# Optimization experiments

Hardware: AMD Instinct MI355X
Metric: run time of the kernel (lower is better)

The kernel has to match this reference:

```python
import jax, jax.numpy as jnp
import numpy as np
from jax import lax

LEAK = 0.2
EPS = 1e-5
T = 20  # sequence_length


def _lrelu(x):
    return jnp.where(x >= 0, x, LEAK * x)


def _deconv(x, w, stride=2, k=4, p=1):
    # PyTorch ConvTranspose2d(weight [in,out,kH,kW], stride=2, pad=1) equivalent:
    # flip kernel spatially, swap in/out channels, use lhs_dilation.
    wt = jnp.flip(w, (2, 3)).transpose(1, 0, 2, 3)  # OIHW
    pad = k - 1 - p
    return lax.conv_general_dilated(
        x, wt, window_strides=(1, 1), padding=[(pad, pad), (pad, pad)],
        lhs_dilation=(stride, stride),
        dimension_numbers=('NCHW', 'OIHW', 'NCHW'))


def _bn(x, g, b):
    # BatchNorm2d, training mode (batch statistics, biased variance)
    m = x.mean((0, 2, 3), keepdims=True)
    v = x.var((0, 2, 3), keepdims=True)
    return (x - m) * lax.rsqrt(v + EPS) * g[None, :, None, None] + b[None, :, None, None]


def setup_inputs() -> dict:
    B, CD, MD, H, FF = 64, 128, 128, 256, 512
    ks = jax.random.split(jax.random.key(0), 32)
    rn = lambda k, sh, s=0.02: (s * jax.random.normal(k, sh)).astype(jnp.float32)
    return {
        'z_content': jax.random.normal(ks[0], (B, CD), jnp.float32),
        'z_motion': jax.random.normal(ks[1], (B, MD), jnp.float32),
        'W_h': rn(ks[2], (H, CD + MD)), 'b_h': jnp.zeros((H,), jnp.float32),
        'W_c': rn(ks[3], (H, CD + MD)), 'b_c': jnp.zeros((H,), jnp.float32),
        'W_ih': rn(ks[4], (4 * H, H)), 'W_hh': rn(ks[5], (4 * H, H)),
        'b_ih': jnp.zeros((4 * H,), jnp.float32), 'b_hh': jnp.zeros((4 * H,), jnp.float32),
        'W_f': rn(ks[6], (FF, H)), 'b_f': jnp.zeros((FF,), jnp.float32),
        'init_in': rn(ks[7], (1, H), 0.1),
        'fc_W': rn(ks[8], (256 * 4 * 4, FF + CD)), 'fc_b': jnp.zeros((256 * 16,), jnp.float32),
        'w0': rn(ks[9], (256, 128, 4, 4)), 'g0': jnp.ones((128,), jnp.float32), 'be0': jnp.zeros((128,), jnp.float32),
        'w1': rn(ks[10], (128, 64, 4, 4)), 'g1': jnp.ones((64,), jnp.float32), 'be1': jnp.zeros((64,), jnp.float32),
        'w2': rn(ks[11], (64, 32, 4, 4)), 'g2': jnp.ones((32,), jnp.float32), 'be2': jnp.zeros((32,), jnp.float32),
        'wf': rn(ks[12], (32, 1, 4, 4)), 'bf': jnp.zeros((1,), jnp.float32),
    }


def reference(z_content, z_motion, W_h, b_h, W_c, b_c, W_ih, W_hh, b_ih, b_hh,
              W_f, b_f, init_in, fc_W, fc_b, w0, g0, be0, w1, g1, be1,
              w2, g2, be2, wf, bf):
    B = z_content.shape[0]
    z = jnp.concatenate([z_content, z_motion], axis=-1)
    h0 = z @ W_h.T + b_h  # [B,H]
    c0 = z @ W_c.T + b_c
    x0 = jnp.broadcast_to(init_in, (B, init_in.shape[1]))
    bias = b_ih + b_hh

    def step(carry, _):
        x, h, c = carry
        gates = x @ W_ih.T + h @ W_hh.T + bias  # [B,4H], torch gate order i,f,g,o
        i, f, g, o = jnp.split(gates, 4, axis=-1)
        c_new = jax.nn.sigmoid(f) * c + jax.nn.sigmoid(i) * jnp.tanh(g)
        h_new = jax.nn.sigmoid(o) * jnp.tanh(c_new)
        return (h_new, h_new, c_new), h_new

    _, outs = lax.scan(step, (x0, h0, c0), None, length=T)  # [T,B,H]
    outs = outs.transpose(1, 0, 2)  # [B,T,H]

    ff = _lrelu(outs @ W_f.T + b_f)  # [B,T,FF]
    zc = jnp.broadcast_to(z_content[:, None, :], (B, T, z_content.shape[1]))
    feat = jnp.concatenate([ff, zc], axis=-1).reshape(B * T, -1)  # [B*T, FF+CD]

    h = _lrelu(feat @ fc_W.T + fc_b).reshape(B * T, 256, 4, 4)
    h = _lrelu(_bn(_deconv(h, w0), g0, be0))   # [B*T,128,8,8]
    h = _lrelu(_bn(_deconv(h, w1), g1, be1))   # [B*T,64,16,16]
    h = _lrelu(_bn(_deconv(h, w2), g2, be2))   # [B*T,32,32,32]
    out = jax.nn.sigmoid(_deconv(h, wf) + bf[None, :, None, None])  # [B*T,1,64,64]
    return out.reshape(B, T, *out.shape[1:])
```

## Files before the change

kernel.cpp:

```cpp
#include <hip/hip_runtime.h>
#include <hip/hip_bf16.h>
#include <math.h>

typedef __hip_bfloat16 bf16;
typedef __attribute__((ext_vector_type(8))) short bf16x8;
typedef __attribute__((ext_vector_type(4))) float f32x4;
typedef __attribute__((ext_vector_type(2))) float f32x2;

#define LRELU(v) ((v) > 0.f ? (v) : 0.2f*(v))

__device__ __forceinline__ float sig_f(float x){ return 1.f/(1.f + __expf(-x)); }
__device__ __forceinline__ float tanh_f(float x){
  float ax = fabsf(x);
  float e = __expf(-2.f*ax);
  float t = (1.f - e)/(1.f + e);
  return x >= 0.f ? t : -t;
}
__device__ __forceinline__ ushort bfbits(float v){
  bf16 b = __float2bfloat16(v);
  return *(ushort*)&b;
}
__device__ __forceinline__ uint bfpack(float a, float b){
  return (uint)bfbits(a) | ((uint)bfbits(b) << 16);
}
__device__ __forceinline__ float bflo(uint u){ return __uint_as_float(u << 16); }
__device__ __forceinline__ float bfhi(uint u){ return __uint_as_float(u & 0xffff0000u); }

__global__ void k_tobf16(const float* __restrict__ src, ushort* __restrict__ dst, int n){
  int i = blockIdx.x*256 + threadIdx.x;
  if (i < n) dst[i] = bfbits(src[i]);
}

__global__ void k_transpose(const float* __restrict__ src, float* __restrict__ dst, int R, int C){
  __shared__ float t[32][33];
  int c0 = blockIdx.x*32, r0 = blockIdx.y*32;
  int tx = threadIdx.x, ty = threadIdx.y;
  #pragma unroll
  for (int i = 0; i < 4; ++i)
    t[ty+8*i][tx] = src[(size_t)(r0+ty+8*i)*C + c0+tx];
  __syncthreads();
  #pragma unroll
  for (int i = 0; i < 4; ++i)
    dst[(size_t)(c0+ty+8*i)*R + r0+tx] = t[tx][ty+8*i];
}

__global__ void k_w4prep(const float* __restrict__ Wih, const float* __restrict__ Whh,
                         uint4* __restrict__ Whq8, uint4* __restrict__ Wsq8,
                         float* __restrict__ stats){
  int k4 = blockIdx.x, j = threadIdx.x;
  if (k4 < 2) { int i = k4*256 + j; if (i < 448) stats[i] = 0.f; }
  uint h4[4], s4[4];
  #pragma unroll
  for (int d = 0; d < 4; ++d) {
    int k = 4*k4 + d;
    float hi = Whh[j*256+k],       hf = Whh[(256+j)*256+k];
    float hg = Whh[(512+j)*256+k], ho = Whh[(768+j)*256+k];
    float ii = Wih[j*256+k],       iff = Wih[(256+j)*256+k];
    float ig = Wih[(512+j)*256+k], io = Wih[(768+j)*256+k];
    int lo = __builtin_amdgcn_cvt_pk_fp8_f32(hi, hf, 0, false);
    h4[d] = (uint)__builtin_amdgcn_cvt_pk_fp8_f32(hg, ho, lo, true);
    lo = __builtin_amdgcn_cvt_pk_fp8_f32(hi+ii, hf+iff, 0, false);
    s4[d] = (uint)__builtin_amdgcn_cvt_pk_fp8_f32(hg+ig, ho+io, lo, true);
  }
  Whq8[k4*256+j] = make_uint4(h4[0], h4[1], h4[2], h4[3]);
  Wsq8[k4*256+j] = make_uint4(s4[0], s4[1], s4[2], s4[3]);
}

__global__ void k_xgbias(const float* __restrict__ Wih, const float* __restrict__ b_ih,
                         const float* __restrict__ b_hh, const float* __restrict__ init_in,
                         float4* __restrict__ xg4, float4* __restrict__ bias4){
  int b = blockIdx.x, t = threadIdx.x;
  float v = init_in[t];
  float p0 = v * Wih[b*256 + t];
  float p1 = v * Wih[(256+b)*256 + t];
  float p2 = v * Wih[(512+b)*256 + t];
  float p3 = v * Wih[(768+b)*256 + t];
  #pragma unroll
  for (int o = 32; o; o >>= 1) {
    p0 += __shfl_xor(p0, o); p1 += __shfl_xor(p1, o);
    p2 += __shfl_xor(p2, o); p3 += __shfl_xor(p3, o);
  }
  __shared__ float4 red[4];
  int lane = t & 63, wid = t >> 6;
  if (lane == 0) red[wid] = make_float4(p0,p1,p2,p3);
  __syncthreads();
  if (t == 0) {
    float4 bi = make_float4(b_ih[b]+b_hh[b], b_ih[256+b]+b_hh[256+b],
                            b_ih[512+b]+b_hh[512+b], b_ih[768+b]+b_hh[768+b]);
    bias4[b] = bi;
    float4 a = bi;
    #pragma unroll
    for (int w = 0; w < 4; ++w) { a.x += red[w].x; a.y += red[w].y; a.z += red[w].z; a.w += red[w].w; }
    xg4[b] = a;
  }
}

__global__ __launch_bounds__(256) void k_h0c0(const float* __restrict__ zc, const float* __restrict__ zm,
                      const float* __restrict__ WhT, const float* __restrict__ WcT,
                      const float* __restrict__ b_h, const float* __restrict__ b_c,
                      float* __restrict__ h, float* __restrict__ c){
  __shared__ float zs[256];
  int b = blockIdx.x, j = threadIdx.x;
  zs[j] = (j < 128) ? zc[b*128 + j] : zm[b*128 + (j-128)];
  __syncthreads();
  float ah = b_h[j], ac = b_c[j];
  #pragma unroll 4
  for (int k = 0; k < 256; ++k) {
    float zv = zs[k];
    ah = fmaf(zv, WhT[k*256 + j], ah);
    ac = fmaf(zv, WcT[k*256 + j], ac);
  }
  h[b*256+j] = ah; c[b*256+j] = ac;
}

__global__ __launch_bounds__(1024) void k_lstm_all(
    const uint4* __restrict__ Whq8, const uint4* __restrict__ Wsq8,
    const float4* __restrict__ xg4, const float4* __restrict__ bias4,
    const float* __restrict__ h0, const float* __restrict__ c0,
    ushort* __restrict__ outsb){
  __shared__ float hs[256];
  __shared__ float4 part[3][256];
  const int b = blockIdx.x, tid = threadIdx.x;
  const int j = tid & 255, kq = tid >> 8;
  float cj = 0.f;
  if (kq == 0) { hs[j] = h0[b*256 + j]; cj = c0[b*256 + j]; }
  __syncthreads();
  for (int t = 0; t < 20; ++t) {
    const uint4* __restrict__ Wp = ((t == 0) ? Whq8 : Wsq8) + (size_t)(kq*16)*256 + j;
    float4 a = make_float4(0.f, 0.f, 0.f, 0.f);
    #pragma unroll 8
    for (int kk = 0; kk < 16; ++kk) {
      uint4 wv = Wp[(size_t)kk*256];
      const float* __restrict__ hb = &hs[kq*64 + 4*kk];
      {
        f32x2 pif = __builtin_amdgcn_cvt_pk_f32_fp8((int)wv.x, false);
        f32x2 pgo = __builtin_amdgcn_cvt_pk_f32_fp8((int)wv.x, true);
        float hv = hb[0];
        a.x = fmaf(hv, pif[0], a.x); a.y = fmaf(hv, pif[1], a.y);
        a.z = fmaf(hv, pgo[0], a.z); a.w = fmaf(hv, pgo[1], a.w);
      }
      {
        f32x2 pif = __builtin_amdgcn_cvt_pk_f32_fp8((int)wv.y, false);
        f32x2 pgo = __builtin_amdgcn_cvt_pk_f32_fp8((int)wv.y, true);
        float hv = hb[1];
        a.x = fmaf(hv, pif[0], a.x); a.y = fmaf(hv, pif[1], a.y);
        a.z = fmaf(hv, pgo[0], a.z); a.w = fmaf(hv, pgo[1], a.w);
      }
      {
        f32x2 pif = __builtin_amdgcn_cvt_pk_f32_fp8((int)wv.z, false);
        f32x2 pgo = __builtin_amdgcn_cvt_pk_f32_fp8((int)wv.z, true);
        float hv = hb[2];
        a.x = fmaf(hv, pif[0], a.x); a.y = fmaf(hv, pif[1], a.y);
        a.z = fmaf(hv, pgo[0], a.z); a.w = fmaf(hv, pgo[1], a.w);
      }
      {
        f32x2 pif = __builtin_amdgcn_cvt_pk_f32_fp8((int)wv.w, false);
        f32x2 pgo = __builtin_amdgcn_cvt_pk_f32_fp8((int)wv.w, true);
        float hv = hb[3];
        a.x = fmaf(hv, pif[0], a.x); a.y = fmaf(hv, pif[1], a.y);
        a.z = fmaf(hv, pgo[0], a.z); a.w = fmaf(hv, pgo[1], a.w);
      }
    }
    if (kq) part[kq-1][j] = a;
    __syncthreads();
    if (kq == 0) {
      float4 p1 = part[0][j], p2 = part[1][j], p3 = part[2][j];
      float4 bb = (t == 0) ? xg4[j] : bias4[j];
      a.x += p1.x + p2.x + p3.x + bb.x;
      a.y += p1.y + p2.y + p3.y + bb.y;
      a.z += p1.z + p2.z + p3.z + bb.z;
      a.w += p1.w + p2.w + p3.w + bb.w;
      float ig = sig_f(a.x), fg = sig_f(a.y), gg = tanh_f(a.z), og = sig_f(a.w);
      cj = fmaf(fg, cj, ig*gg);
      float hj = og * tanh_f(cj);
      outsb[(b*20 + t)*256 + j] = bfbits(hj);
      hs[j] = hj;
    }
    __syncthreads();
  }
}

__global__ void k_zc(const float* __restrict__ zc, ushort* __restrict__ featb){
  int e = blockIdx.x*256 + threadIdx.x;
  int r = e >> 7, c = e & 127;
  featb[r*640 + 512 + c] = bfbits(zc[(r/20)*128 + c]);
}

__global__ __launch_bounds__(256) void k_ff_m(
    const ushort* __restrict__ A, const ushort* __restrict__ W,
    const float* __restrict__ bias, ushort* __restrict__ C)
{
  constexpr int K = 256, BK = 64, NK = K/BK, BM = 128, BN = 64;
  constexpr int RS = 72;
  constexpr int NCF = BN/16;
  constexpr int AC = 4, WC = 2;

  __shared__ __align__(16) ushort Al[2][BM*RS];
  __shared__ __align__(16) ushort Wl[2][BN*RS];

  const int tid = threadIdx.x;
  const int col0 = blockIdx.x * BN, row0 = blockIdx.y * BM;
  const int w = tid >> 6, l = tid & 63, lm = l & 15, lk = l >> 4;

  f32x4 acc[NCF][2];
  #pragma unroll
  for (int m = 0; m < NCF; ++m)
    #pragma unroll
    for (int s = 0; s < 2; ++s)
      acc[m][s] = (f32x4){0.f,0.f,0.f,0.f};

  uint4 ar[AC], wr[WC];

  #define LOADG(kt) { \
    _Pragma("unroll") \
    for (int i = 0; i < AC; ++i) { \
      int chunk = tid + i*256; \
      int rl = chunk >> 3, kc = chunk & 7; \
      ar[i] = *(const uint4*)&A[(size_t)(row0+rl)*K + (kt)*BK + kc*8]; \
    } \
    _Pragma("unroll") \
    for (int i = 0; i < WC; ++i) { \
      int chunk = tid + i*256; \
      int co = chunk >> 3, kc = chunk & 7; \
      wr[i] = *(const uint4*)&W[(size_t)(col0+co)*K + (kt)*BK + kc*8]; \
    } }

  #define STOREL(buf) { \
    _Pragma("unroll") \
    for (int i = 0; i < AC; ++i) { \
      int chunk = tid + i*256; \
      int rl = chunk >> 3, kc = chunk & 7; \
      *(uint4*)&Al[buf][rl*RS + kc*8] = ar[i]; \
    } \
    _Pragma("unroll") \
    for (int i = 0; i < WC; ++i) { \
      int chunk = tid + i*256; \
      int co = chunk >> 3, kc = chunk & 7; \
      *(uint4*)&Wl[buf][co*RS + kc*8] = wr[i]; \
    } }

  LOADG(0);
  STOREL(0);
  int cur = 0;
  for (int kt = 0; kt < NK; ++kt) {
    if (kt + 1 < NK) LOADG(kt + 1);
    __syncthreads();
    #pragma unroll
    for (int kf = 0; kf < 2; ++kf) {
      bf16x8 bfr[2];
      #pragma unroll
      for (int s = 0; s < 2; ++s)
        bfr[s] = *(bf16x8*)&Al[cur][(w*32 + s*16 + lm)*RS + kf*32 + lk*8];
      #pragma unroll
      for (int m = 0; m < NCF; ++m) {
        bf16x8 afr = *(bf16x8*)&Wl[cur][(m*16 + lm)*RS + kf*32 + lk*8];
        acc[m][0] = __builtin_amdgcn_mfma_f32_16x16x32_bf16(afr, bfr[0], acc[m][0], 0, 0, 0);
        acc[m][1] = __builtin_amdgcn_mfma_f32_16x16x32_bf16(afr, bfr[1], acc[m][1], 0, 0, 0);
      }
    }
    if (kt + 1 < NK) STOREL(cur ^ 1);
    cur ^= 1;
  }

  #pragma unroll
  for (int m = 0; m < NCF; ++m) {
    #pragma unroll
    for (int s = 0; s < 2; ++s) {
      int row = row0 + w*32 + s*16 + lm;
      f32x4 v = acc[m][s];
      int u0 = col0 + m*16 + lk*4;
      union { ushort u[4]; uint2 q; } pk;
      #pragma unroll
      for (int j = 0; j < 4; ++j)
        pk.u[j] = bfbits(LRELU(v[j] + bias[u0+j]));
      *(uint2*)&C[(size_t)row*640 + u0] = pk.q;
    }
  }
  #undef LOADG
  #undef STOREL
}

__global__ __launch_bounds__(256) void k_gemm_fc_m(
    const ushort* __restrict__ A, const ushort* __restrict__ W,
    const float* __restrict__ bias, ushort* __restrict__ C)
{
  constexpr int K = 640, BK = 64, NK = K/BK, BM = 128, BN = 64;
  constexpr int RS = 72;
  constexpr int NCF = BN/16;
  constexpr int AC = 4, WC = 2;

  __shared__ __align__(16) ushort Al[2][BM*RS];
  __shared__ __align__(16) ushort Wl[2][BN*RS];

  const int tid = threadIdx.x;
  const int col0 = blockIdx.x * BN, row0 = blockIdx.y * BM;
  const int w = tid >> 6, l = tid & 63, lm = l & 15, lk = l >> 4;

  f32x4 acc[NCF][2];
  #pragma unroll
  for (int m = 0; m < NCF; ++m)
    #pragma unroll
    for (int s = 0; s < 2; ++s)
      acc[m][s] = (f32x4){0.f,0.f,0.f,0.f};

  uint4 ar[AC], wr[WC];

  #define LOADG(kt) { \
    _Pragma("unroll") \
    for (int i = 0; i < AC; ++i) { \
      int chunk = tid + i*256; \
      int rl = chunk >> 3, kc = chunk & 7; \
      ar[i] = *(const uint4*)&A[(size_t)(row0+rl)*K + (kt)*BK + kc*8]; \
    } \
    _Pragma("unroll") \
    for (int i = 0; i < WC; ++i) { \
      int chunk = tid + i*256; \
      int co = chunk >> 3, kc = chunk & 7; \
      wr[i] = *(const uint4*)&W[(size_t)(col0+co)*K + (kt)*BK + kc*8]; \
    } }

  #define STOREL(buf) { \
    _Pragma("unroll") \
    for (int i = 0; i < AC; ++i) { \
      int chunk = tid + i*256; \
      int rl = chunk >> 3, kc = chunk & 7; \
      *(uint4*)&Al[buf][rl*RS + kc*8] = ar[i]; \
    } \
    _Pragma("unroll") \
    for (int i = 0; i < WC; ++i) { \
      int chunk = tid + i*256; \
      int co = chunk >> 3, kc = chunk & 7; \
      *(uint4*)&Wl[buf][co*RS + kc*8] = wr[i]; \
    } }

  LOADG(0);
  STOREL(0);
  int cur = 0;
  for (int kt = 0; kt < NK; ++kt) {
    if (kt + 1 < NK) LOADG(kt + 1);
    __syncthreads();
    #pragma unroll
    for (int kf = 0; kf < 2; ++kf) {
      bf16x8 bfr[2];
      #pragma unroll
      for (int s = 0; s < 2; ++s)
        bfr[s] = *(bf16x8*)&Al[cur][(w*32 + s*16 + lm)*RS + kf*32 + lk*8];
      #pragma unroll
      for (int m = 0; m < NCF; ++m) {
        bf16x8 afr = *(bf16x8*)&Wl[cur][(m*16 + lm)*RS + kf*32 + lk*8];
        acc[m][0] = __builtin_amdgcn_mfma_f32_16x16x32_bf16(afr, bfr[0], acc[m][0], 0, 0, 0);
        acc[m][1] = __builtin_amdgcn_mfma_f32_16x16x32_bf16(afr, bfr[1], acc[m][1], 0, 0, 0);
      }
    }
    if (kt + 1 < NK) STOREL(cur ^ 1);
    cur ^= 1;
  }

  #pragma unroll
  for (int m = 0; m < NCF; ++m) {
    #pragma unroll
    for (int s = 0; s < 2; ++s) {
      int row = row0 + w*32 + s*16 + lm;
      f32x4 v = acc[m][s];
      #pragma unroll
      for (int j = 0; j < 4; ++j) {
        int u = col0 + m*16 + lk*4 + j;
        float val = LRELU(v[j] + bias[u]);
        C[((size_t)row << 12) + ((size_t)(u & 15) << 8) + (u >> 4)] = bfbits(val);
      }
    }
  }
  #undef LOADG
  #undef STOREL
}

template<int CI, int CO>
__global__ void k_wprep_im(const float* __restrict__ w, ushort* __restrict__ wpn){
  constexpr int K = 4*CI, KF = K/32, MMW2 = CO/16;
  int e = blockIdx.x*256 + threadIdx.x;
  if (e >= 16*CI*CO) return;
  int j  = e & 7;
  int lk = (e >> 3) & 3;
  int lm = (e >> 5) & 15;
  int r3 = e >> 9;
  int kf = r3 % KF; int r4 = r3 / KF;
  int m  = r4 % MMW2; int p = r4 / MMW2;
  int k  = kf*32 + lk*8 + j;
  int t  = k / CI, ci = k % CI;
  int co = m*16 + lm;
  int py = p >> 1, px = p & 1, dy = t >> 1, dx = t & 1;
  int ky = (py ? 0 : 1) + 2*dy;
  int kx = (px ? 0 : 1) + 2*dx;
  wpn[e] = bfbits(w[((ci*CO + co)*4 + ky)*4 + kx]);
}

__global__ void k_wfprep(const float* __restrict__ wf, ushort* __restrict__ wfb){
  int e = blockIdx.x*256 + threadIdx.x;
  if (e < 512) {
    int t = e >> 5, ci = e & 31;
    wfb[t*32 + ci] = bfbits(wf[ci*16 + t]);
  }
}

template<int CI, int CO, int HI>
__global__ __launch_bounds__(256) void k_dcv(
    const ushort* __restrict__ in, const ushort* __restrict__ wp,
    ushort* __restrict__ out, float* __restrict__ gsum, float* __restrict__ gsq)
{
  constexpr int WI = HI, HO = 2*HI, WO = 2*WI;
  constexpr int K = 4*CI, BK = 64, NK = K/BK, KFT = K/32;
  constexpr int BSP = 128;
  constexpr int RS = 72;
  constexpr int NCF = CO/32;
  constexpr int COH = CO/2;
  constexpr int AC = BSP/32;

  __shared__ __align__(16) ushort Al[2][BSP*RS];
  __shared__ float s_sum[COH], s_sq[COH];

  const int tid = threadIdx.x;
  const int sp0 = blockIdx.x * BSP;
  const int p  = blockIdx.y;
  const int coz = blockIdx.z;
  const int py = p >> 1, px = p & 1;
  const int w  = tid >> 6, l = tid & 63;
  const int lm = l & 15, lk = l >> 4;

  if (tid < COH) { s_sum[tid] = 0.f; s_sq[tid] = 0.f; }

  f32x4 acc[NCF][2];
  #pragma unroll
  for (int m = 0; m < NCF; ++m)
    #pragma unroll
    for (int s = 0; s < 2; ++s)
      acc[m][s] = (f32x4){0.f,0.f,0.f,0.f};

  uint4 ar[AC];
  const ushort* wpb = wp + (size_t)(p*(CO/16) + coz*NCF)*KFT*512;

  #define LOADT(kt) { \
    int t = ((kt)*BK)/CI, ci0 = ((kt)*BK)%CI; \
    int dy = t >> 1, dx = t & 1; \
    _Pragma("unroll") \
    for (int i = 0; i < AC; ++i) { \
      int chunk = tid + i*256; \
      int rl = chunk >> 3, kc = chunk & 7; \
      int r = sp0 + rl; \
      int n = r / (HI*WI), rem = r % (HI*WI); \
      int oy = rem / WI, ox = rem % WI; \
      int iy = oy + py - dy, ix = ox + px - dx; \
      if ((unsigned)iy < (unsigned)HI && (unsigned)ix < (unsigned)WI) \
        ar[i] = *(const uint4*)&in[((((size_t)n*HI + iy)*WI + ix)*CI) + ci0 + kc*8]; \
      else ar[i] = make_uint4(0,0,0,0); \
    } }

  #define STORET(buf) { \
    _Pragma("unroll") \
    for (int i = 0; i < AC; ++i) { \
      int chunk = tid + i*256; \
      int rl = chunk >> 3, kc = chunk & 7; \
      *(uint4*)&Al[buf][rl*RS + kc*8] = ar[i]; \
    } }

  LOADT(0);
  STORET(0);
  int cur = 0;
  for (int kt = 0; kt < NK; ++kt) {
    if (kt + 1 < NK) LOADT(kt + 1);
    __syncthreads();
    #pragma unroll
    for (int kf = 0; kf < 2; ++kf) {
      const int ktg = kt*2 + kf;
      bf16x8 bfr[2];
      #pragma unroll
      for (int s = 0; s < 2; ++s)
        bfr[s] = *(bf16x8*)&Al[cur][(w*32 + s*16 + lm)*RS + kf*32 + lk*8];
      #pragma unroll
      for (int m = 0; m < NCF; ++m) {
        bf16x8 afr = *(const bf16x8*)&wpb[((size_t)m*KFT + ktg)*512 + lm*32 + lk*8];
        acc[m][0] = __builtin_amdgcn_mfma_f32_16x16x32_bf16(afr, bfr[0], acc[m][0], 0, 0, 0);
        acc[m][1] = __builtin_amdgcn_mfma_f32_16x16x32_bf16(afr, bfr[1], acc[m][1], 0, 0, 0);
      }
    }
    if (kt + 1 < NK) STORET(cur ^ 1);
    cur ^= 1;
  }

  #pragma unroll
  for (int m = 0; m < NCF; ++m) {
    float s1[4] = {0,0,0,0}, s2[4] = {0,0,0,0};
    #pragma unroll
    for (int s = 0; s < 2; ++s) {
      f32x4 v = acc[m][s];
      #pragma unroll
      for (int j = 0; j < 4; ++j) { s1[j] += v[j]; s2[j] += v[j]*v[j]; }
    }
    #pragma unroll
    for (int j = 0; j < 4; ++j) {
      float a = s1[j], b = s2[j];
      #pragma unroll
      for (int o = 1; o < 16; o <<= 1) { a += __shfl_xor(a, o); b += __shfl_xor(b, o); }
      if (lm == 0) {
        atomicAdd(&s_sum[m*16 + lk*4 + j], a);
        atomicAdd(&s_sq [m*16 + lk*4 + j], b);
      }
    }
  }
  #pragma unroll
  for (int s = 0; s < 2; ++s) {
    int sp = sp0 + w*32 + s*16 + lm;
    int n = sp / (HI*WI), rem = sp % (HI*WI);
    int y = 2*(rem / WI) + py, x = 2*(rem % WI) + px;
    size_t ob = (((size_t)n*HO + y)*WO + x)*CO + coz*COH + lk*4;
    #pragma unroll
    for (int m = 0; m < NCF; ++m) {
      f32x4 v = acc[m][s];
      union { ushort u[4]; uint2 q; } pk;
      pk.u[0] = bfbits(v[0]); pk.u[1] = bfbits(v[1]);
      pk.u[2] = bfbits(v[2]); pk.u[3] = bfbits(v[3]);
      *(uint2*)&out[ob + m*16] = pk.q;
    }
  }
  __syncthreads();
  for (int cc = tid; cc < COH; cc += 256) {
    atomicAdd(&gsum[coz*COH + cc], s_sum[cc]);
    atomicAdd(&gsq[coz*COH + cc],  s_sq[cc]);
  }
  #undef LOADT
  #undef STORET
}

template<int CI, int CO, int HI>
__global__ __launch_bounds__(512) void k_dcvim(
    const ushort* __restrict__ in, const ushort* __restrict__ wp,
    const float* __restrict__ gsumP, const float* __restrict__ gsqP,
    const float* __restrict__ gP, const float* __restrict__ beP, float invNP,
    ushort* __restrict__ out, float* __restrict__ gsum, float* __restrict__ gsq)
{
  constexpr int WI = HI, HO = 2*HI, WO = 2*WI;
  constexpr int K = 4*CI;
  constexpr int KF = K/32;
  constexpr int PAD = HI + 2;
  constexpr int CICH = CI/8;
  constexpr int MMW2 = CO/16;
  constexpr int SFTH = HI*WI/32;

  __shared__ __align__(16) ushort Ain[PAD*PAD*CI];
  __shared__ float s_sum[CO], s_sq[CO];
  __shared__ float s_scale[CI], s_shift[CI];

  const int tid = threadIdx.x;
  const int n = blockIdx.x;
  const int w = tid >> 6, l = tid & 63, lm = l & 15, lk = l >> 4;
  const int p = w >> 1, py = p >> 1, px = p & 1, ph = w & 1;

  if (tid < CO) { s_sum[tid] = 0.f; s_sq[tid] = 0.f; }
  if (tid >= 512-CI) {
    int c = tid - (512-CI);
    float m = gsumP[c]*invNP;
    float v = gsqP[c]*invNP - m*m;
    float sc = gP[c]*rsqrtf(v + 1e-5f);
    s_scale[c] = sc;
    s_shift[c] = beP[c] - m*sc;
  }
  __syncthreads();

  const ushort* inb = in + (size_t)n * HI * WI * CI;
  constexpr int NPCH = PAD*PAD*CICH;
  for (int e = tid; e < NPCH; e += 512) {
    int ci8 = e % CICH; int sp = e / CICH;
    int c = sp % PAD, r = sp / PAD;
    int chS = ci8 ^ (c & 7);
    if (r >= 1 && r <= HI && c >= 1 && c <= WI) {
      uint4 u = *(const uint4*)&inb[(((size_t)(r-1)*WI + (c-1))*CI) + ci8*8];
      int ci0 = ci8*8;
      float4 sc0 = *(const float4*)&s_scale[ci0];
      float4 sc1 = *(const float4*)&s_scale[ci0+4];
      float4 sh0 = *(const float4*)&s_shift[ci0];
      float4 sh1 = *(const float4*)&s_shift[ci0+4];
      float v0 = LRELU(fmaf(bflo(u.x), sc0.x, sh0.x));
      float v1 = LRELU(fmaf(bfhi(u.x), sc0.y, sh0.y));
      float v2 = LRELU(fmaf(bflo(u.y), sc0.z, sh0.z));
      float v3 = LRELU(fmaf(bfhi(u.y), sc0.w, sh0.w));
      float v4 = LRELU(fmaf(bflo(u.z), sc1.x, sh1.x));
      float v5 = LRELU(fmaf(bfhi(u.z), sc1.y, sh1.y));
      float v6 = LRELU(fmaf(bflo(u.w), sc1.z, sh1.z));
      float v7 = LRELU(fmaf(bfhi(u.w), sc1.w, sh1.w));
      uint4 o;
      o.x = (uint)bfpack(v0, v1);
      o.y = (uint)bfpack(v2, v3);
      o.z = (uint)bfpack(v4, v5);
      o.w = (uint)bfpack(v6, v7);
      ((uint4*)Ain)[(r*PAD + c)*CICH + chS] = o;
    } else {
      ((uint4*)Ain)[(r*PAD + c)*CICH + chS] = make_uint4(0,0,0,0);
    }
  }
  __syncthreads();

  f32x4 acc[MMW2][SFTH];
  #pragma unroll
  for (int m = 0; m < MMW2; ++m)
    #pragma unroll
    for (int sf = 0; sf < SFTH; ++sf)
      acc[m][sf] = (f32x4){0.f,0.f,0.f,0.f};

  const ushort* wpb = wp + (size_t)(p*MMW2)*KF*512;
  #pragma unroll
  for (int kf = 0; kf < KF; ++kf) {
    const int t = (kf*32)/CI, cib = (kf*32)%CI;
    const int dy = t >> 1, dx = t & 1;
    bf16x8 afr[MMW2];
    #pragma unroll
    for (int m = 0; m < MMW2; ++m)
      afr[m] = *(const bf16x8*)&wpb[((size_t)m*KF + kf)*512 + lm*32 + lk*8];
    const int ch = (cib >> 3) + lk;
    #pragma unroll
    for (int sf = 0; sf < SFTH; ++sf) {
      int s = (ph*SFTH + sf)*16 + lm;
      int y = s / WI, x = s % WI;
      int r = y + py - dy + 1, c = x + px - dx + 1;
      bf16x8 bfr = *(const bf16x8*)&Ain[((r*PAD + c)*CICH + (ch ^ (c & 7)))*8];
      #pragma unroll
      for (int m = 0; m < MMW2; ++m)
        acc[m][sf] = __builtin_amdgcn_mfma_f32_16x16x32_bf16(afr[m], bfr, acc[m][sf], 0, 0, 0);
    }
  }

  float s1[MMW2][4], s2[MMW2][4];
  #pragma unroll
  for (int m = 0; m < MMW2; ++m)
    #pragma unroll
    for (int j = 0; j < 4; ++j) { s1[m][j] = 0.f; s2[m][j] = 0.f; }

  #pragma unroll
  for (int sf = 0; sf < SFTH; ++sf) {
    int s = (ph*SFTH + sf)*16 + lm;
    int y = 2*(s / WI) + py, x = 2*(s % WI) + px;
    size_t ob = (((size_t)n*HO + y)*WO + x)*CO + lk*4;
    #pragma unroll
    for (int m = 0; m < MMW2; ++m) {
      f32x4 v = acc[m][sf];
      union { ushort u[4]; uint2 q; } pk;
      #pragma unroll
      for (int j = 0; j < 4; ++j) {
        pk.u[j] = bfbits(v[j]);
        s1[m][j] += v[j];
        s2[m][j] += v[j]*v[j];
      }
      *(uint2*)&out[ob + m*16] = pk.q;
    }
  }

  #pragma unroll
  for (int m = 0; m < MMW2; ++m) {
    #pragma unroll
    for (int j = 0; j < 4; ++j) {
      float a = s1[m][j], b = s2[m][j];
      #pragma unroll
      for (int o = 1; o < 16; o <<= 1) { a += __shfl_xor(a, o); b += __shfl_xor(b, o); }
      if (lm == 0) {
        atomicAdd(&s_sum[m*16 + lk*4 + j], a);
        atomicAdd(&s_sq [m*16 + lk*4 + j], b);
      }
    }
  }

  __syncthreads();
  for (int cc = tid; cc < CO; cc += 512) {
    atomicAdd(&gsum[cc], s_sum[cc]);
    atomicAdd(&gsq[cc],  s_sq[cc]);
  }
}

__global__ __launch_bounds__(256) void k_final(
    const ushort* __restrict__ in, const ushort* __restrict__ wfb,
    const float* __restrict__ gsumP, const float* __restrict__ gsqP,
    const float* __restrict__ gP, const float* __restrict__ beP, float invNP,
    const float* __restrict__ bfb, float* __restrict__ outp)
{
  constexpr int CI=32, HI=32, WI=32, HO=64, WO=64, SPLIT=4, HOq=HO/SPLIT;
  constexpr int RMAX = 10;
  constexpr int DP = 20;
  __shared__ float Dl[RMAX*32*DP];
  __shared__ float s_scale[CI], s_shift[CI];

  const int tid = threadIdx.x, bid = blockIdx.x;
  const int n = bid % 1280, q = bid / 1280;
  const int y0 = q * HOq;
  const int rows_lo = max(0, y0/2 - 1);
  const int rows_hi = min(HI-1, (y0 + HOq)/2);
  const int nrows = rows_hi - rows_lo + 1;

  if (tid < CI) {
    float m = gsumP[tid]*invNP;
    float v = gsqP[tid]*invNP - m*m;
    float sc = gP[tid]*rsqrtf(v + 1e-5f);
    s_scale[tid] = sc;
    s_shift[tid] = beP[tid] - m*sc;
  }
  __syncthreads();

  const int w = tid >> 6, l = tid & 63, lm = l & 15, lk = l >> 4;
  const bf16x8 afr = *(const bf16x8*)&wfb[lm*32 + lk*8];
  const float4 sc0 = *(const float4*)&s_scale[lk*8];
  const float4 sc1 = *(const float4*)&s_scale[lk*8+4];
  const float4 sh0 = *(const float4*)&s_shift[lk*8];
  const float4 sh1 = *(const float4*)&s_shift[lk*8+4];

  const ushort* inb = in + (size_t)n * HI * WI * CI;
  const int ngrp = nrows * 2;
  for (int g = w; g < ngrp; g += 4) {
    int px = g*16 + lm;
    int rl = px >> 5, ix = px & 31;
    uint4 u = *(const uint4*)&inb[(((size_t)(rows_lo+rl)*WI + ix)*CI) + lk*8];
    float v0 = LRELU(fmaf(bflo(u.x), sc0.x, sh0.x));
    float v1 = LRELU(fmaf(bfhi(u.x), sc0.y, sh0.y));
    float v2 = LRELU(fmaf(bflo(u.y), sc0.z, sh0.z));
    float v3 = LRELU(fmaf(bfhi(u.y), sc0.w, sh0.w));
    float v4 = LRELU(fmaf(bflo(u.z), sc1.x, sh1.x));
    float v5 = LRELU(fmaf(bfhi(u.z), sc1.y, sh1.y));
    float v6 = LRELU(fmaf(bflo(u.w), sc1.z, sh1.z));
    float v7 = LRELU(fmaf(bfhi(u.w), sc1.w, sh1.w));
    union { uint uu[4]; bf16x8 v; } pk;
    pk.uu[0] = bfpack(v0, v1);
    pk.uu[1] = bfpack(v2, v3);
    pk.uu[2] = bfpack(v4, v5);
    pk.uu[3] = bfpack(v6, v7);
    f32x4 d = __builtin_amdgcn_mfma_f32_16x16x32_bf16(afr, pk.v, (f32x4){0.f,0.f,0.f,0.f}, 0, 0, 0);
    *(f32x4*)&Dl[px*DP + lk*4] = d;
  }
  __syncthreads();

  const float b0 = bfb[0];
  #pragma unroll
  for (int i = 0; i < (HOq*WO)/256; ++i) {
    int e = tid + i*256;
    int oy = e >> 6, x = e & 63;
    int y = y0 + oy;
    int kya = (y + 1) & 1, iya = (y + 1) >> 1;
    int kxa = (x + 1) & 1, ixa = (x + 1) >> 1;
    float acc = b0;
    #pragma unroll
    for (int dy = 0; dy < 2; ++dy) {
      int iy = iya - dy, ky = kya + 2*dy;
      if (iy < 0 || iy >= HI) continue;
      #pragma unroll
      for (int dx = 0; dx < 2; ++dx) {
        int ix = ixa - dx, kx = kxa + 2*dx;
        if (ix < 0 || ix >= WI) continue;
        acc += Dl[((iy - rows_lo)*WI + ix)*DP + (ky*4 + kx)];
      }
    }
    outp[(size_t)n*HO*WO + y*WO + x] = 1.f/(1.f + __expf(-acc));
  }
}

extern "C" void kernel_launch(void* const* d_in, const int* in_sizes, int n_in,
                              void* d_out, int out_size, void* d_ws, size_t ws_size,
                              hipStream_t stream) {
  const float* z_content = (const float*)d_in[0];
  const float* z_motion  = (const float*)d_in[1];
  const float* W_h  = (const float*)d_in[2];
  const float* b_h  = (const float*)d_in[3];
  const float* W_c  = (const float*)d_in[4];
  const float* b_c  = (const float*)d_in[5];
  const float* W_ih = (const float*)d_in[6];
  const float* W_hh = (const float*)d_in[7];
  const float* b_ih = (const float*)d_in[8];
  const float* b_hh = (const float*)d_in[9];
  const float* W_f  = (const float*)d_in[10];
  const float* b_f  = (const float*)d_in[11];
  const float* init_in = (const float*)d_in[12];
  const float* fc_W = (const float*)d_in[13];
  const float* fc_b = (const float*)d_in[14];
  const float* w0 = (const float*)d_in[15];
  const float* g0 = (const float*)d_in[16];
  const float* be0 = (const float*)d_in[17];
  const float* w1 = (const float*)d_in[18];
  const float* g1 = (const float*)d_in[19];
  const float* be1 = (const float*)d_in[20];
  const float* w2 = (const float*)d_in[21];
  const float* g2 = (const float*)d_in[22];
  const float* be2 = (const float*)d_in[23];
  const float* wf = (const float*)d_in[24];
  const float* bf_ = (const float*)d_in[25];

  const size_t P_BYTES = 10631168;
  const size_t X_OFF   = P_BYTES;
  const size_t X_BYTES = 83886080;
  const size_t Y_OFF   = X_OFF + X_BYTES;
  const size_t NEED    = Y_OFF + 41943040;
  if (ws_size < NEED) return;

  float* ws = (float*)d_ws;
  char*  wsb = (char*)d_ws;
  float* sum0 = ws + 0;        float* sq0 = ws + 128;
  float* sum1 = ws + 256;      float* sq1 = ws + 320;
  float* sum2 = ws + 384;      float* sq2 = ws + 416;
  float4* xg4   = (float4*)(ws + 1024);
  float4* bias4 = (float4*)(ws + 2048);
  float* h    = ws + 3072;
  float* c    = ws + 19456;
  ushort* outsb = (ushort*)(ws + 35840);
  float* WhT  = ws + 199680;
  float* WcT  = ws + 265216;
  uint4* Whq8 = (uint4*)(ws + 330752);
  uint4* Wsq8 = (uint4*)(ws + 592896);
  ushort* wp0 = (ushort*)(ws + 855040);
  ushort* wp1 = (ushort*)(ws + 1117184);
  ushort* wp2 = (ushort*)(ws + 1182720);
  ushort* wfb = (ushort*)(ws + 1199104);
  ushort* wpff = (ushort*)(ws + 1199616);
  ushort* featb = (ushort*)(ws + 1265152);

  ushort* wpfc = (ushort*)(wsb + X_OFF);
  ushort* out0 = (ushort*)(wsb + X_OFF);
  ushort* out2 = (ushort*)(wsb + X_OFF);
  ushort* h1   = (ushort*)(wsb + Y_OFF);
  ushort* out1 = (ushort*)(wsb + Y_OFF);

  dim3 tb(32,8);
  k_transpose<<<dim3(8,8),   tb, 0, stream>>>(W_h,  WhT, 256, 256);
  k_transpose<<<dim3(8,8),   tb, 0, stream>>>(W_c,  WcT, 256, 256);
  k_tobf16<<<10240, 256, 0, stream>>>(fc_W, wpfc, 2621440);
  k_tobf16<<<512, 256, 0, stream>>>(W_f, wpff, 131072);
  k_w4prep<<<64, 256, 0, stream>>>(W_ih, W_hh, Whq8, Wsq8, ws);
  k_xgbias<<<256, 256, 0, stream>>>(W_ih, b_ih, b_hh, init_in, xg4, bias4);
  k_h0c0<<<64, 256, 0, stream>>>(z_content, z_motion, WhT, WcT, b_h, b_c, h, c);
  k_wprep_im<256,128><<<2048, 256, 0, stream>>>(w0, wp0);
  k_wprep_im<128,64><<<512, 256, 0, stream>>>(w1, wp1);
  k_wprep_im<64,32><<<128, 256, 0, stream>>>(w2, wp2);
  k_wfprep<<<2, 256, 0, stream>>>(wf, wfb);

  k_lstm_all<<<64, 1024, 0, stream>>>(Whq8, Wsq8, xg4, bias4, h, c, outsb);

  k_ff_m<<<dim3(8, 10), 256, 0, stream>>>(outsb, wpff, b_f, featb);
  k_zc<<<640, 256, 0, stream>>>(z_content, featb);
  k_gemm_fc_m<<<dim3(64, 10), 256, 0, stream>>>(featb, wpfc, fc_b, h1);

  k_dcv<256,128,4><<<dim3(160,4,2), 256, 0, stream>>>(h1, wp0, out0, sum0, sq0);
  k_dcvim<128,64,8><<<1280, 512, 0, stream>>>(out0, wp1, sum0, sq0, g0, be0, 1.f/81920.f, out1, sum1, sq1);
  k_dcvim<64,32,16><<<1280, 512, 0, stream>>>(out1, wp2, sum1, sq1, g1, be1, 1.f/327680.f, out2, sum2, sq2);
  k_final<<<5120, 256, 0, stream>>>(out2, wfb, sum2, sq2, g2, be2, 1.f/1310720.f, bf_, (float*)d_out);
}
```

Baseline: 444.6 us.

## Split deconv blocks by output parity, stage weights in LDS, loop over images

The two middle deconv+BN kernels now assign one output parity phase per block (blockIdx.y) and process G=8 images per block in sequence. Each block stages its parity's weight slice in shared memory once and reuses it across the images. The 8 waves split (tile, channel-group) pairs instead of parity/half-plane pairs. BN statistics accumulate in registers across the images, which cuts the number of atomics per block. In exchange, each input image is loaded and normalized four times (once per parity block), LDS use grows, and the grid shrinks from 1280 to 640 blocks.

```diff
diff --git a/kernel.cpp b/kernel.cpp
--- a/kernel.cpp
+++ b/kernel.cpp
@@ -530,29 +530,31 @@
   #undef STORET
 }
 
-template<int CI, int CO, int HI>
-__global__ __launch_bounds__(512) void k_dcvim(
+template<int CI, int CO, int HI, int G, int MINW>
+__global__ __launch_bounds__(512, MINW) void k_dcvw(
     const ushort* __restrict__ in, const ushort* __restrict__ wp,
     const float* __restrict__ gsumP, const float* __restrict__ gsqP,
     const float* __restrict__ gP, const float* __restrict__ beP, float invNP,
     ushort* __restrict__ out, float* __restrict__ gsum, float* __restrict__ gsq)
 {
   constexpr int WI = HI, HO = 2*HI, WO = 2*WI;
-  constexpr int K = 4*CI;
-  constexpr int KF = K/32;
+  constexpr int KF = 4*CI/32;
   constexpr int PAD = HI + 2;
   constexpr int CICH = CI/8;
   constexpr int MMW2 = CO/16;
-  constexpr int SFTH = HI*WI/32;
-
+  constexpr int NPX = HI*WI;
+  constexpr int TILES = NPX/16;
+  constexpr int PPW = TILES*MMW2/8;
+
+  __shared__ __align__(16) ushort Wl[MMW2*KF*512];
   __shared__ __align__(16) ushort Ain[PAD*PAD*CI];
+  __shared__ float s_scale[CI], s_shift[CI];
   __shared__ float s_sum[CO], s_sq[CO];
-  __shared__ float s_scale[CI], s_shift[CI];
 
   const int tid = threadIdx.x;
-  const int n = blockIdx.x;
+  const int g0 = blockIdx.x * G;
+  const int p = blockIdx.y, py = p >> 1, px = p & 1;
   const int w = tid >> 6, l = tid & 63, lm = l & 15, lk = l >> 4;
-  const int p = w >> 1, py = p >> 1, px = p & 1, ph = w & 1;
 
   if (tid < CO) { s_sum[tid] = 0.f; s_sq[tid] = 0.f; }
   if (tid >= 512-CI) {
@@ -563,100 +565,103 @@
     s_scale[c] = sc;
     s_shift[c] = beP[c] - m*sc;
   }
+  {
+    const uint4* wpb4 = (const uint4*)(wp + (size_t)(p*MMW2)*KF*512);
+    constexpr int WCH = MMW2*KF*64;
+    for (int e = tid; e < WCH; e += 512)
+      ((uint4*)Wl)[e] = wpb4[e];
+  }
   __syncthreads();
 
-  const ushort* inb = in + (size_t)n * HI * WI * CI;
-  constexpr int NPCH = PAD*PAD*CICH;
-  for (int e = tid; e < NPCH; e += 512) {
-    int ci8 = e % CICH; int sp = e / CICH;
-    int c = sp % PAD, r = sp / PAD;
-    int chS = ci8 ^ (c & 7);
-    if (r >= 1 && r <= HI && c >= 1 && c <= WI) {
-      uint4 u = *(const uint4*)&inb[(((size_t)(r-1)*WI + (c-1))*CI) + ci8*8];
-      int ci0 = ci8*8;
-      float4 sc0 = *(const float4*)&s_scale[ci0];
-      float4 sc1 = *(const float4*)&s_scale[ci0+4];
-      float4 sh0 = *(const float4*)&s_shift[ci0];
-      float4 sh1 = *(const float4*)&s_shift[ci0+4];
-      float v0 = LRELU(fmaf(bflo(u.x), sc0.x, sh0.x));
-      float v1 = LRELU(fmaf(bfhi(u.x), sc0.y, sh0.y));
-      float v2 = LRELU(fmaf(bflo(u.y), sc0.z, sh0.z));
-      float v3 = LRELU(fmaf(bfhi(u.y), sc0.w, sh0.w));
-      float v4 = LRELU(fmaf(bflo(u.z), sc1.x, sh1.x));
-      float v5 = LRELU(fmaf(bfhi(u.z), sc1.y, sh1.y));
-      float v6 = LRELU(fmaf(bflo(u.w), sc1.z, sh1.z));
-      float v7 = LRELU(fmaf(bfhi(u.w), sc1.w, sh1.w));
-      uint4 o;
-      o.x = (uint)bfpack(v0, v1);
-      o.y = (uint)bfpack(v2, v3);
-      o.z = (uint)bfpack(v4, v5);
-      o.w = (uint)bfpack(v6, v7);
-      ((uint4*)Ain)[(r*PAD + c)*CICH + chS] = o;
-    } else {
-      ((uint4*)Ain)[(r*PAD + c)*CICH + chS] = make_uint4(0,0,0,0);
-    }
-  }
-  __syncthreads();
-
-  f32x4 acc[MMW2][SFTH];
-  #pragma unroll
-  for (int m = 0; m < MMW2; ++m)
-    #pragma unroll
-    for (int sf = 0; sf < SFTH; ++sf)
-      acc[m][sf] = (f32x4){0.f,0.f,0.f,0.f};
-
-  const ushort* wpb = wp + (size_t)(p*MMW2)*KF*512;
-  #pragma unroll
-  for (int kf = 0; kf < KF; ++kf) {
-    const int t = (kf*32)/CI, cib = (kf*32)%CI;
-    const int dy = t >> 1, dx = t & 1;
-    bf16x8 afr[MMW2];
-    #pragma unroll
-    for (int m = 0; m < MMW2; ++m)
-      afr[m] = *(const bf16x8*)&wpb[((size_t)m*KF + kf)*512 + lm*32 + lk*8];
-    const int ch = (cib >> 3) + lk;
-    #pragma unroll
-    for (int sf = 0; sf < SFTH; ++sf) {
-      int s = (ph*SFTH + sf)*16 + lm;
-      int y = s / WI, x = s % WI;
-      int r = y + py - dy + 1, c = x + px - dx + 1;
-      bf16x8 bfr = *(const bf16x8*)&Ain[((r*PAD + c)*CICH + (ch ^ (c & 7)))*8];
-      #pragma unroll
-      for (int m = 0; m < MMW2; ++m)
-        acc[m][sf] = __builtin_amdgcn_mfma_f32_16x16x32_bf16(afr[m], bfr, acc[m][sf], 0, 0, 0);
-    }
-  }
-
-  float s1[MMW2][4], s2[MMW2][4];
-  #pragma unroll
-  for (int m = 0; m < MMW2; ++m)
-    #pragma unroll
-    for (int j = 0; j < 4; ++j) { s1[m][j] = 0.f; s2[m][j] = 0.f; }
-
-  #pragma unroll
-  for (int sf = 0; sf < SFTH; ++sf) {
-    int s = (ph*SFTH + sf)*16 + lm;
-    int y = 2*(s / WI) + py, x = 2*(s % WI) + px;
-    size_t ob = (((size_t)n*HO + y)*WO + x)*CO + lk*4;
-    #pragma unroll
-    for (int m = 0; m < MMW2; ++m) {
-      f32x4 v = acc[m][sf];
-      union { ushort u[4]; uint2 q; } pk;
+  float st1[PPW][4], st2[PPW][4];
+  #pragma unroll
+  for (int i = 0; i < PPW; ++i)
+    #pragma unroll
+    for (int j = 0; j < 4; ++j) { st1[i][j] = 0.f; st2[i][j] = 0.f; }
+
+  for (int gi = 0; gi < G; ++gi) {
+    const int n = g0 + gi;
+    const ushort* inb = in + (size_t)n * HI * WI * CI;
+    constexpr int NPCH = PAD*PAD*CICH;
+    for (int e = tid; e < NPCH; e += 512) {
+      int ci8 = e % CICH; int sp = e / CICH;
+      int c = sp % PAD, r = sp / PAD;
+      int chS = ci8 ^ (c & 7);
+      if (r >= 1 && r <= HI && c >= 1 && c <= WI) {
+        uint4 u = *(const uint4*)&inb[(((size_t)(r-1)*WI + (c-1))*CI) + ci8*8];
+        int ci0 = ci8*8;
+        float4 sc0 = *(const float4*)&s_scale[ci0];
+        float4 sc1 = *(const float4*)&s_scale[ci0+4];
+        float4 sh0 = *(const float4*)&s_shift[ci0];
+        float4 sh1 = *(const float4*)&s_shift[ci0+4];
+        float v0 = LRELU(fmaf(bflo(u.x), sc0.x, sh0.x));
+        float v1 = LRELU(fmaf(bfhi(u.x), sc0.y, sh0.y));
+        float v2 = LRELU(fmaf(bflo(u.y), sc0.z, sh0.z));
+        float v3 = LRELU(fmaf(bfhi(u.y), sc0.w, sh0.w));
+        float v4 = LRELU(fmaf(bflo(u.z), sc1.x, sh1.x));
+        float v5 = LRELU(fmaf(bfhi(u.z), sc1.y, sh1.y));
+        float v6 = LRELU(fmaf(bflo(u.w), sc1.z, sh1.z));
+        float v7 = LRELU(fmaf(bfhi(u.w), sc1.w, sh1.w));
+        uint4 o;
+        o.x = (uint)bfpack(v0, v1);
+        o.y = (uint)bfpack(v2, v3);
+        o.z = (uint)bfpack(v4, v5);
+        o.w = (uint)bfpack(v6, v7);
+        ((uint4*)Ain)[(r*PAD + c)*CICH + chS] = o;
+      } else {
+        ((uint4*)Ain)[(r*PAD + c)*CICH + chS] = make_uint4(0,0,0,0);
+      }
+    }
+    __syncthreads();
+
+    f32x4 acc[PPW];
+    #pragma unroll
+    for (int i = 0; i < PPW; ++i) acc[i] = (f32x4){0.f,0.f,0.f,0.f};
+
+    #pragma unroll
+    for (int kf = 0; kf < KF; ++kf) {
+      const int t = (kf*32)/CI, cib = (kf*32)%CI;
+      const int dy = t >> 1, dx = t & 1;
+      const int ch = (cib >> 3) + lk;
+      #pragma unroll
+      for (int i = 0; i < PPW; ++i) {
+        const int q = w*PPW + i;
+        const int tl = q / MMW2, m = q % MMW2;
+        int s = tl*16 + lm;
+        int y = s / WI, x = s % WI;
+        int r = y + py - dy + 1, c = x + px - dx + 1;
+        bf16x8 bfr = *(const bf16x8*)&Ain[((r*PAD + c)*CICH + (ch ^ (c & 7)))*8];
+        bf16x8 afr = *(const bf16x8*)&Wl[((size_t)m*KF + kf)*512 + lm*32 + lk*8];
+        acc[i] = __builtin_amdgcn_mfma_f32_16x16x32_bf16(afr, bfr, acc[i], 0, 0, 0);
+      }
+    }
+
+    #pragma unroll
+    for (int i = 0; i < PPW; ++i) {
+      const int q = w*PPW + i;
+      const int tl = q / MMW2, m = q % MMW2;
+      int s = tl*16 + lm;
+      int y = 2*(s / WI) + py, x = 2*(s % WI) + px;
+      size_t ob = (((size_t)n*HO + y)*WO + x)*CO + m*16 + lk*4;
+      f32x4 v = acc[i];
+      union { ushort u[4]; uint2 qq; } pk;
       #pragma unroll
       for (int j = 0; j < 4; ++j) {
         pk.u[j] = bfbits(v[j]);
-        s1[m][j] += v[j];
-        s2[m][j] += v[j]*v[j];
-      }
-      *(uint2*)&out[ob + m*16] = pk.q;
-    }
-  }
-
-  #pragma unroll
-  for (int m = 0; m < MMW2; ++m) {
+        st1[i][j] += v[j];
+        st2[i][j] += v[j]*v[j];
+      }
+      *(uint2*)&out[ob] = pk.qq;
+    }
+    __syncthreads();
+  }
+
+  #pragma unroll
+  for (int i = 0; i < PPW; ++i) {
+    const int m = (w*PPW + i) % MMW2;
     #pragma unroll
     for (int j = 0; j < 4; ++j) {
-      float a = s1[m][j], b = s2[m][j];
+      float a = st1[i][j], b = st2[i][j];
       #pragma unroll
       for (int o = 1; o < 16; o <<= 1) { a += __shfl_xor(a, o); b += __shfl_xor(b, o); }
       if (lm == 0) {
@@ -665,7 +670,6 @@
       }
     }
   }
-
   __syncthreads();
   for (int cc = tid; cc < CO; cc += 512) {
     atomicAdd(&gsum[cc], s_sum[cc]);
@@ -840,7 +844,7 @@
   k_gemm_fc_m<<<dim3(64, 10), 256, 0, stream>>>(featb, wpfc, fc_b, h1);
 
   k_dcv<256,128,4><<<dim3(160,4,2), 256, 0, stream>>>(h1, wp0, out0, sum0, sq0);
-  k_dcvim<128,64,8><<<1280, 512, 0, stream>>>(out0, wp1, sum0, sq0, g0, be0, 1.f/81920.f, out1, sum1, sq1);
-  k_dcvim<64,32,16><<<1280, 512, 0, stream>>>(out1, wp2, sum1, sq1, g1, be1, 1.f/327680.f, out2, sum2, sq2);
+  k_dcvw<128,64,8,8,2><<<dim3(160,4), 512, 0, stream>>>(out0, wp1, sum0, sq0, g0, be0, 1.f/81920.f, out1, sum1, sq1);
+  k_dcvw<64,32,16,8,4><<<dim3(160,4), 512, 0, stream>>>(out1, wp2, sum1, sq1, g1, be1, 1.f/327680.f, out2, sum2, sq2);
   k_final<<<5120, 256, 0, stream>>>(out2, wfb, sum2, sq2, g2, be2, 1.f/1310720.f, bf_, (float*)d_out);
 }
```

After: 485.8 us. 9.3% more time.
